# Optimization experiments

Measured on AMD Instinct MI355X. Metric: run time of the kernel, lower is better.

The kernel has to match this reference:

```python
import jax, jax.numpy as jnp
import numpy as np

B, S, F = 16, 511, 128           # batch, input seq len, n_features
D, H, NB = 512, 8, 6             # embedding_dim, n_heads, n_blocks
DH = D // H                      # d_head
MLP = 4 * D                      # mlp_ratio=4 hard-coded in FxtBlock
OUT = 1                          # out_d
T = S + 1                        # tokens incl. cls
EPS = 1e-5                       # torch LayerNorm default eps


def pos_emb(seq_len, d):
    # matches get_positional_embeddings: sin for even j, cos for odd j (with j-1 exponent)
    i = np.arange(seq_len, dtype=np.float32)[:, None]
    j = np.arange(d)
    je = np.where(j % 2 == 0, j, j - 1).astype(np.float32)
    ang = i / (10000.0 ** (je / d))
    pe = np.where(j % 2 == 0, np.sin(ang), np.cos(ang))
    return jnp.asarray(pe, jnp.float32)


def layernorm(x, g, b):
    m = jnp.mean(x, axis=-1, keepdims=True)
    v = jnp.mean((x - m) ** 2, axis=-1, keepdims=True)
    return (x - m) * jax.lax.rsqrt(v + EPS) * g + b


def setup_inputs() -> dict:
    key = jax.random.key(0)
    ks = jax.random.split(key, 12)
    g = lambda k, shape: jax.random.normal(k, shape, jnp.float32) * 0.02
    return {
        "src": jax.random.normal(ks[0], (B, S, F), jnp.float32),
        "emb_W": g(ks[1], (F, D)), "emb_b": jnp.zeros((D,), jnp.float32),
        "cls_tok": jax.random.uniform(ks[2], (1, D), jnp.float32),
        "ln1_g": jnp.ones((NB, D), jnp.float32), "ln1_b": jnp.zeros((NB, D), jnp.float32),
        "Wq": g(ks[3], (NB, H, DH, DH)), "bq": jnp.zeros((NB, H, DH), jnp.float32),
        "Wk": g(ks[4], (NB, H, DH, DH)), "bk": jnp.zeros((NB, H, DH), jnp.float32),
        "Wv": g(ks[5], (NB, H, DH, DH)), "bv": jnp.zeros((NB, H, DH), jnp.float32),
        "ln2_g": jnp.ones((NB, D), jnp.float32), "ln2_b": jnp.zeros((NB, D), jnp.float32),
        "W1": g(ks[6], (NB, D, MLP)), "b1": jnp.zeros((NB, MLP), jnp.float32),
        "W2": g(ks[7], (NB, MLP, D)), "b2": jnp.zeros((NB, D), jnp.float32),
        "head_W": g(ks[8], (D, OUT)), "head_b": jnp.zeros((OUT,), jnp.float32),
    }


def reference(src, emb_W, emb_b, cls_tok, ln1_g, ln1_b, Wq, bq, Wk, bk, Wv, bv,
              ln2_g, ln2_b, W1, b1, W2, b2, head_W, head_b):
    b = src.shape[0]
    x = src @ emb_W + emb_b                                    # [B,S,D]
    cls = jnp.broadcast_to(cls_tok[None], (b, 1, D))
    x = jnp.concatenate([cls, x], axis=1) + pos_emb(T, D)[None]  # [B,T,D]
    scale = 1.0 / jnp.sqrt(jnp.float32(DH))
    for i in range(NB):
        h = layernorm(x, ln1_g[i], ln1_b[i])
        hh = h.reshape(b, T, H, DH)
        q = jnp.einsum('bthd,hde->bhte', hh, Wq[i]) + bq[i][None, :, None, :]
        k = jnp.einsum('bthd,hde->bhte', hh, Wk[i]) + bk[i][None, :, None, :]
        v = jnp.einsum('bthd,hde->bhte', hh, Wv[i]) + bv[i][None, :, None, :]
        attn = jax.nn.softmax(jnp.einsum('bhse,bhte->bhst', q, k) * scale, axis=-1)
        o = jnp.einsum('bhst,bhte->bhse', attn, v)             # [B,H,T,DH]
        x = x + o.transpose(0, 2, 1, 3).reshape(b, T, D)
        h2 = layernorm(x, ln2_g[i], ln2_b[i])
        x = x + (jax.nn.gelu(h2 @ W1[i] + b1[i], approximate=False) @ W2[i] + b2[i])
    return jax.nn.sigmoid(x[:, 0] @ head_W + head_b)           # [B,OUT]
```

## Files before the change

### kernel.cpp

```cpp
#include <hip/hip_runtime.h>
#include <hip/hip_bf16.h>
#include <math.h>

#define B 16
#define S 511
#define F 128
#define D 512
#define H 8
#define NB 6
#define DH 64
#define MLPD 2048
#define T 512
#define EPS 1e-5f

typedef unsigned short ushort;
typedef __attribute__((ext_vector_type(8))) short short8;
typedef __attribute__((ext_vector_type(4))) float floatx4;

__device__ __forceinline__ ushort f2bf(float f) {
    union { float f; unsigned u; } cv; cv.f = f;
    unsigned r = (cv.u + 0x7fff + ((cv.u >> 16) & 1)) >> 16;
    return (ushort)r;
}

__global__ void castsrc_kernel(const float* __restrict__ src, ushort* __restrict__ srcb) {
    int row = blockIdx.x;
    int t = row & (T - 1), b = row >> 9;
    int tid = threadIdx.x;
    ushort v = 0;
    if (t > 0) v = f2bf(src[((size_t)b * S + (t - 1)) * F + tid]);
    srcb[(size_t)row * F + tid] = v;
}

__global__ void wtrans_kernel(const float* __restrict__ W,
                              ushort* __restrict__ Wt,
                              int K, int N) {
    int kb = blockIdx.x * 32, nb = blockIdx.y * 32, mat = blockIdx.z;
    __shared__ float tile[32][33];
    int tid = threadIdx.x;
    int c = tid & 31, r0 = tid >> 5;
    const float* Wm = W + (size_t)mat * K * N;
    ushort* Wtm = Wt + (size_t)mat * K * N;
    #pragma unroll
    for (int l = 0; l < 4; ++l) {
        int r = r0 + l * 8;
        tile[r][c] = Wm[(size_t)(kb + r) * N + nb + c];
    }
    __syncthreads();
    #pragma unroll
    for (int l = 0; l < 4; ++l) {
        int r = r0 + l * 8;
        Wtm[(size_t)(nb + r) * K + kb + c] = f2bf(tile[c][r]);
    }
}

__global__ void wtransq_kernel(const float* __restrict__ Wq, const float* __restrict__ Wk,
                               const float* __restrict__ Wv,
                               ushort* __restrict__ WqT, ushort* __restrict__ WkT,
                               ushort* __restrict__ WvT) {
    int mat = blockIdx.x;
    int which = blockIdx.y;
    const float* W = (which == 0 ? Wq : which == 1 ? Wk : Wv) + (size_t)mat * 4096;
    ushort* O = (which == 0 ? WqT : which == 1 ? WkT : WvT) + (size_t)mat * 4096;
    __shared__ float t[64][65];
    int tid = threadIdx.x;
    int r0 = tid >> 6, c = tid & 63;
    #pragma unroll
    for (int l = 0; l < 16; ++l) {
        int row = r0 * 16 + l;
        t[row][c] = W[row * 64 + c];
    }
    __syncthreads();
    #pragma unroll
    for (int l = 0; l < 16; ++l) {
        int row = r0 * 16 + l;
        O[row * 64 + c] = f2bf(t[c][row]);
    }
}

__device__ __forceinline__ void gload_lds16(const ushort* g, ushort* l) {
    __builtin_amdgcn_global_load_lds((const __attribute__((address_space(1))) unsigned int*)g,
                                     (__attribute__((address_space(3))) unsigned int*)l,
                                     16, 0, 0);
}

__global__ __launch_bounds__(256) void embed_gemm(const ushort* __restrict__ A,
                                                  const ushort* __restrict__ Bt,
                                                  const float* __restrict__ emb_b,
                                                  const float* __restrict__ cls_tok,
                                                  float* __restrict__ x) {
    __shared__ ushort As[64 * 32];
    __shared__ ushort Bs[64 * 32];
    int tid = threadIdx.x;
    int lane = tid & 63;
    int w = __builtin_amdgcn_readfirstlane(tid >> 6);
    int quad = lane >> 4, l15 = lane & 15;
    int wr = (w >> 1) * 32, wc = (w & 1) * 32;
    int m0 = blockIdx.x * 64, n0 = blockIdx.y * 64;

    floatx4 acc[2][2];
    #pragma unroll
    for (int i = 0; i < 2; ++i)
        #pragma unroll
        for (int j = 0; j < 2; ++j) acc[i][j] = (floatx4)0.f;

    int lrow = lane >> 2;
    int lk = (lane & 3) * 8;
    const ushort* Ag = A + (size_t)(m0 + 16 * w + lrow) * F + lk;
    const ushort* Bg = Bt + (size_t)(n0 + 16 * w + lrow) * F + lk;
    ushort* AsW = &As[16 * w * 32];
    ushort* BsW = &Bs[16 * w * 32];
    int fa = l15 * 32 + quad * 8;

    for (int kt = 0; kt < F; kt += 32) {
        gload_lds16(Ag + kt, AsW);
        gload_lds16(Bg + kt, BsW);
        __syncthreads();
        short8 af[2], bf[2];
        #pragma unroll
        for (int i = 0; i < 2; ++i) af[i] = *(const short8*)&As[(wr + 16 * i) * 32 + fa];
        #pragma unroll
        for (int j = 0; j < 2; ++j) bf[j] = *(const short8*)&Bs[(wc + 16 * j) * 32 + fa];
        #pragma unroll
        for (int i = 0; i < 2; ++i)
            #pragma unroll
            for (int j = 0; j < 2; ++j)
                acc[i][j] = __builtin_amdgcn_mfma_f32_16x16x32_bf16(af[i], bf[j], acc[i][j], 0, 0, 0);
        __syncthreads();
    }

    const float LOG1E4 = 9.210340371976184f;
    int rbase = (lane >> 4) * 4;
    int cidx = lane & 15;
    #pragma unroll
    for (int j = 0; j < 2; ++j) {
        int gc = n0 + wc + 16 * j + cidx;
        float je = (float)(gc & ~1);
        float freq = expf(-(je / (float)D) * LOG1E4);
        float ebv = emb_b[gc];
        float clsv = cls_tok[gc];
        bool odd = (gc & 1);
        #pragma unroll
        for (int i = 0; i < 2; ++i) {
            int gr = m0 + wr + 16 * i + rbase;
            #pragma unroll
            for (int reg = 0; reg < 4; ++reg) {
                int row = gr + reg;
                int t = row & (T - 1);
                float ang = (float)t * freq;
                float pe = odd ? cosf(ang) : sinf(ang);
                float val = (t == 0) ? (clsv + pe) : (acc[i][j][reg] + ebv + pe);
                x[(size_t)row * D + gc] = val;
            }
        }
    }
}

__global__ __launch_bounds__(256) void ln_kernel(const float* __restrict__ xin,
                                                 const float* __restrict__ g,
                                                 const float* __restrict__ bb,
                                                 ushort* __restrict__ out) {
    int lane = threadIdx.x & 63;
    int row = blockIdx.x * 4 + (threadIdx.x >> 6);
    const float* xr = xin + (size_t)row * D + lane * 8;
    float4 a0 = *(const float4*)xr;
    float4 a1 = *(const float4*)(xr + 4);
    float s = a0.x + a0.y + a0.z + a0.w + a1.x + a1.y + a1.z + a1.w;
    #pragma unroll
    for (int off = 1; off < 64; off <<= 1) s += __shfl_xor(s, off);
    float mean = s * (1.0f / (float)D);
    float d0 = a0.x - mean, d1 = a0.y - mean, d2 = a0.z - mean, d3 = a0.w - mean;
    float d4 = a1.x - mean, d5 = a1.y - mean, d6 = a1.z - mean, d7 = a1.w - mean;
    float sq = d0*d0 + d1*d1 + d2*d2 + d3*d3 + d4*d4 + d5*d5 + d6*d6 + d7*d7;
    #pragma unroll
    for (int off = 1; off < 64; off <<= 1) sq += __shfl_xor(sq, off);
    float rstd = rsqrtf(sq * (1.0f / (float)D) + EPS);
    const float* gp = g + lane * 8;
    const float* bp = bb + lane * 8;
    float4 g0 = *(const float4*)gp, g1 = *(const float4*)(gp + 4);
    float4 b0 = *(const float4*)bp, b1 = *(const float4*)(bp + 4);
    short8 o;
    o[0] = (short)f2bf(d0 * rstd * g0.x + b0.x);
    o[1] = (short)f2bf(d1 * rstd * g0.y + b0.y);
    o[2] = (short)f2bf(d2 * rstd * g0.z + b0.z);
    o[3] = (short)f2bf(d3 * rstd * g0.w + b0.w);
    o[4] = (short)f2bf(d4 * rstd * g1.x + b1.x);
    o[5] = (short)f2bf(d5 * rstd * g1.y + b1.y);
    o[6] = (short)f2bf(d6 * rstd * g1.z + b1.z);
    o[7] = (short)f2bf(d7 * rstd * g1.w + b1.w);
    *(short8*)(out + (size_t)row * D + lane * 8) = o;
}

__global__ __launch_bounds__(256) void ln_fuse_kernel(float* __restrict__ x,
                                                      const float* __restrict__ p0,
                                                      const float* __restrict__ p1,
                                                      const float* __restrict__ g,
                                                      const float* __restrict__ bb,
                                                      ushort* __restrict__ out) {
    int lane = threadIdx.x & 63;
    int row = blockIdx.x * 4 + (threadIdx.x >> 6);
    size_t base = (size_t)row * D + lane * 8;
    float* xr = x + base;
    float4 a0 = *(const float4*)xr;
    float4 a1 = *(const float4*)(xr + 4);
    float4 q0 = *(const float4*)(p0 + base);
    float4 q1 = *(const float4*)(p0 + base + 4);
    float4 r0v = *(const float4*)(p1 + base);
    float4 r1v = *(const float4*)(p1 + base + 4);
    a0.x += q0.x + r0v.x; a0.y += q0.y + r0v.y; a0.z += q0.z + r0v.z; a0.w += q0.w + r0v.w;
    a1.x += q1.x + r1v.x; a1.y += q1.y + r1v.y; a1.z += q1.z + r1v.z; a1.w += q1.w + r1v.w;
    *(float4*)xr = a0;
    *(float4*)(xr + 4) = a1;
    float s = a0.x + a0.y + a0.z + a0.w + a1.x + a1.y + a1.z + a1.w;
    #pragma unroll
    for (int off = 1; off < 64; off <<= 1) s += __shfl_xor(s, off);
    float mean = s * (1.0f / (float)D);
    float d0 = a0.x - mean, d1 = a0.y - mean, d2 = a0.z - mean, d3 = a0.w - mean;
    float d4 = a1.x - mean, d5 = a1.y - mean, d6 = a1.z - mean, d7 = a1.w - mean;
    float sq = d0*d0 + d1*d1 + d2*d2 + d3*d3 + d4*d4 + d5*d5 + d6*d6 + d7*d7;
    #pragma unroll
    for (int off = 1; off < 64; off <<= 1) sq += __shfl_xor(sq, off);
    float rstd = rsqrtf(sq * (1.0f / (float)D) + EPS);
    const float* gp = g + lane * 8;
    const float* bp = bb + lane * 8;
    float4 g0 = *(const float4*)gp, g1 = *(const float4*)(gp + 4);
    float4 b0 = *(const float4*)bp, b1 = *(const float4*)(bp + 4);
    short8 o;
    o[0] = (short)f2bf(d0 * rstd * g0.x + b0.x);
    o[1] = (short)f2bf(d1 * rstd * g0.y + b0.y);
    o[2] = (short)f2bf(d2 * rstd * g0.z + b0.z);
    o[3] = (short)f2bf(d3 * rstd * g0.w + b0.w);
    o[4] = (short)f2bf(d4 * rstd * g1.x + b1.x);
    o[5] = (short)f2bf(d5 * rstd * g1.y + b1.y);
    o[6] = (short)f2bf(d6 * rstd * g1.z + b1.z);
    o[7] = (short)f2bf(d7 * rstd * g1.w + b1.w);
    *(short8*)(out + (size_t)row * D + lane * 8) = o;
}

__global__ __launch_bounds__(256) void qkv_kernel(
        const ushort* __restrict__ hb,
        const ushort* __restrict__ WqT, const float* __restrict__ bq,
        const ushort* __restrict__ WkT, const float* __restrict__ bk,
        const ushort* __restrict__ WvT, const float* __restrict__ bv,
        ushort* __restrict__ qo, ushort* __restrict__ ko, ushort* __restrict__ vTo) {
    int m0 = blockIdx.x * 128;
    int hh = blockIdx.y;
    int tid = threadIdx.x;
    int lane = tid & 63;
    int w = __builtin_amdgcn_readfirstlane(tid >> 6);
    int quad = lane >> 4, l15 = lane & 15;

    short8 af[2][2];
    #pragma unroll
    for (int mt = 0; mt < 2; ++mt) {
        const ushort* ab = hb + (size_t)(m0 + w * 32 + mt * 16 + l15) * D + hh * DH + quad * 8;
        af[mt][0] = *(const short8*)(ab);
        af[mt][1] = *(const short8*)(ab + 32);
    }

    floatx4 acc[3][2][4];
    #pragma unroll
    for (int xo = 0; xo < 3; ++xo)
        #pragma unroll
        for (int mt = 0; mt < 2; ++mt)
            #pragma unroll
            for (int nt = 0; nt < 4; ++nt) acc[xo][mt][nt] = (floatx4)0.f;

    #pragma unroll
    for (int xo = 0; xo < 3; ++xo) {
        const ushort* WT = (xo == 0 ? WqT : xo == 1 ? WkT : WvT) + (size_t)hh * 4096;
        #pragma unroll
        for (int nt = 0; nt < 4; ++nt) {
            const ushort* wb = WT + (size_t)(nt * 16 + l15) * 64 + quad * 8;
            short8 bf0 = *(const short8*)(wb);
            short8 bf1 = *(const short8*)(wb + 32);
            #pragma unroll
            for (int mt = 0; mt < 2; ++mt) {
                acc[xo][mt][nt] = __builtin_amdgcn_mfma_f32_16x16x32_bf16(af[mt][0], bf0, acc[xo][mt][nt], 0, 0, 0);
                acc[xo][mt][nt] = __builtin_amdgcn_mfma_f32_16x16x32_bf16(af[mt][1], bf1, acc[xo][mt][nt], 0, 0, 0);
            }
        }
    }

    int bb = m0 >> 9;
    int bh = bb * H + hh;
    #pragma unroll
    for (int mt = 0; mt < 2; ++mt) {
        int trow = m0 + w * 32 + mt * 16 + quad * 4;
        int tt = trow & (T - 1);
        #pragma unroll
        for (int nt = 0; nt < 4; ++nt) {
            int col = nt * 16 + l15;
            float bqv = bq[hh * DH + col];
            float bkv = bk[hh * DH + col];
            float bvv = bv[hh * DH + col];
            #pragma unroll
            for (int reg = 0; reg < 4; ++reg) {
                qo[((size_t)bh * T + tt + reg) * DH + col] = f2bf(acc[0][mt][nt][reg] + bqv);
                ko[((size_t)bh * T + tt + reg) * DH + col] = f2bf(acc[1][mt][nt][reg] + bkv);
                vTo[((size_t)bh * DH + col) * T + tt + reg] = f2bf(acc[2][mt][nt][reg] + bvv);
            }
        }
    }
}

#define PSTRIDE 88
__global__ __launch_bounds__(256) void attn_kernel(const ushort* __restrict__ q,
                                                   const ushort* __restrict__ k,
                                                   const ushort* __restrict__ vT,
                                                   float* __restrict__ x) {
    int bh = blockIdx.x;
    int qt = blockIdx.y;
    int b = bh >> 3, hh = bh & 7;
    int tid = threadIdx.x;
    int lane = tid & 63;
    int w = __builtin_amdgcn_readfirstlane(tid >> 6);
    int quad = lane >> 4, l15 = lane & 15;

    __shared__ __align__(16) ushort smem[22016];
    ushort* Pw = smem + 16384 + w * (16 * PSTRIDE);

    const ushort* qbase = q + ((size_t)bh * T + qt * 64 + w * 16 + l15) * DH + quad * 8;
    short8 Qf0 = *(const short8*)(qbase);
    short8 Qf1 = *(const short8*)(qbase + 32);

    const ushort* kbase = k + (size_t)bh * T * DH;
    const ushort* vbase = vT + (size_t)bh * DH * T;

    int srow = lane >> 2;
    int scol = (lane & 3) * 8;
    const ushort* kg = kbase + (size_t)(w * 16 + srow) * DH + scol;
    const ushort* vg = vbase + (size_t)(w * 16 + srow) * T + scol;
    ushort* ldsK = smem + w * 16 * 32;
    ushort* ldsV = smem + 8192 + w * 16 * 32;

    float l_i[4] = {0.f, 0.f, 0.f, 0.f};
    floatx4 O[4];
    #pragma unroll
    for (int j = 0; j < 4; ++j) O[j] = (floatx4)0.f;

    gload_lds16(kg, ldsK);
    gload_lds16(kg + 32, ldsK + 2048);
    gload_lds16(vg, ldsV);
    gload_lds16(vg + 32, ldsV + 2048);
    __syncthreads();

    for (int kt = 0; kt < T / 64; ++kt) {
        int cur = kt & 1;
        if (kt < T / 64 - 1) {
            int nb = cur ^ 1;
            const ushort* kgn = kg + (size_t)(kt + 1) * 64 * DH;
            const ushort* vgn = vg + (kt + 1) * 64;
            gload_lds16(kgn, ldsK + nb * 4096);
            gload_lds16(kgn + 32, ldsK + nb * 4096 + 2048);
            gload_lds16(vgn, ldsV + nb * 4096);
            gload_lds16(vgn + 32, ldsV + nb * 4096 + 2048);
        }
        const ushort* Kc = smem + cur * 4096;
        const ushort* Vc = smem + 8192 + cur * 4096;

        floatx4 sc[4];
        #pragma unroll
        for (int j = 0; j < 4; ++j) {
            int ro = (j * 16 + l15) * 32 + quad * 8;
            short8 kf0 = *(const short8*)&Kc[ro];
            short8 kf1 = *(const short8*)&Kc[2048 + ro];
            floatx4 s4 = (floatx4)0.f;
            s4 = __builtin_amdgcn_mfma_f32_16x16x32_bf16(Qf0, kf0, s4, 0, 0, 0);
            s4 = __builtin_amdgcn_mfma_f32_16x16x32_bf16(Qf1, kf1, s4, 0, 0, 0);
            sc[j] = s4;
        }
        #pragma unroll
        for (int j = 0; j < 4; ++j) {
            #pragma unroll
            for (int r = 0; r < 4; ++r) {
                float p = __expf(sc[j][r] * 0.125f);
                ushort pb = f2bf(p);
                union { unsigned u; float f; } cv; cv.u = ((unsigned)pb) << 16;
                l_i[r] += cv.f;
                Pw[(quad * 4 + r) * PSTRIDE + j * 16 + l15] = pb;
            }
        }

        short8 af0 = *(const short8*)&Pw[l15 * PSTRIDE + quad * 8];
        short8 af1 = *(const short8*)&Pw[l15 * PSTRIDE + 32 + quad * 8];
        #pragma unroll
        for (int j = 0; j < 4; ++j) {
            int ro = (j * 16 + l15) * 32 + quad * 8;
            short8 vf0 = *(const short8*)&Vc[ro];
            short8 vf1 = *(const short8*)&Vc[2048 + ro];
            O[j] = __builtin_amdgcn_mfma_f32_16x16x32_bf16(af0, vf0, O[j], 0, 0, 0);
            O[j] = __builtin_amdgcn_mfma_f32_16x16x32_bf16(af1, vf1, O[j], 0, 0, 0);
        }
        __syncthreads();
    }

    #pragma unroll
    for (int r = 0; r < 4; ++r) {
        l_i[r] += __shfl_xor(l_i[r], 1);
        l_i[r] += __shfl_xor(l_i[r], 2);
        l_i[r] += __shfl_xor(l_i[r], 4);
        l_i[r] += __shfl_xor(l_i[r], 8);
    }

    float* Ow = (float*)smem + w * 16 * 68;
    #pragma unroll
    for (int r = 0; r < 4; ++r) {
        float rl = 1.0f / l_i[r];
        #pragma unroll
        for (int j = 0; j < 4; ++j)
            Ow[(quad * 4 + r) * 68 + j * 16 + l15] = O[j][r] * rl;
    }
    __syncthreads();
    int r4 = lane >> 4;
    int c16 = lane & 15;
    #pragma unroll
    for (int i = 0; i < 4; ++i) {
        int lrow = i * 4 + r4;
        float4 o = *(const float4*)&Ow[lrow * 68 + c16 * 4];
        int grow = qt * 64 + w * 16 + lrow;
        float* xp = &x[((size_t)(b * T) + grow) * D + hh * DH + c16 * 4];
        float4 xv = *(const float4*)xp;
        xv.x += o.x; xv.y += o.y; xv.z += o.z; xv.w += o.w;
        *(float4*)xp = xv;
    }
}

template<int MODE, int SPLIT>
__global__ __launch_bounds__(256) void mfma_gemm(const ushort* __restrict__ A,
                                                 const ushort* __restrict__ Bt,
                                                 const float* __restrict__ bias,
                                                 void* __restrict__ Cv,
                                                 int M, int N, int K) {
    __shared__ ushort As0[128 * 32];
    __shared__ ushort As1[128 * 32];
    __shared__ ushort Bs0[128 * 32];
    __shared__ ushort Bs1[128 * 32];
    int tid = threadIdx.x;
    int lane = tid & 63;
    int w = __builtin_amdgcn_readfirstlane(tid >> 6);
    int wr = (w >> 1) * 64, wc = (w & 1) * 64;
    int m0 = blockIdx.x * 128, n0 = blockIdx.y * 128;
    int kz = blockIdx.z;
    int kchunk = K / SPLIT;
    int k0 = kz * kchunk, k1 = k0 + kchunk;

    floatx4 acc[4][4];
    #pragma unroll
    for (int i = 0; i < 4; ++i)
        #pragma unroll
        for (int j = 0; j < 4; ++j) acc[i][j] = (floatx4)0.f;

    int lrow = lane >> 2;
    int lk = (lane & 3) * 8;
    const ushort* Ag = A + (size_t)(m0 + 32 * w + lrow) * K + lk;
    const ushort* Bg = Bt + (size_t)(n0 + 32 * w + lrow) * K + lk;
    ushort* As0W = &As0[(32 * w) * 32];
    ushort* As1W = &As1[(32 * w) * 32];
    ushort* Bs0W = &Bs0[(32 * w) * 32];
    ushort* Bs1W = &Bs1[(32 * w) * 32];
    int fa = (lane & 15) * 32 + (lane >> 4) * 8;

    for (int kt = k0; kt < k1; kt += 64) {
        gload_lds16(Ag + kt, As0W);
        gload_lds16(Ag + kt + (size_t)16 * K, As0W + 16 * 32);
        gload_lds16(Ag + kt + 32, As1W);
        gload_lds16(Ag + kt + 32 + (size_t)16 * K, As1W + 16 * 32);
        gload_lds16(Bg + kt, Bs0W);
        gload_lds16(Bg + kt + (size_t)16 * K, Bs0W + 16 * 32);
        gload_lds16(Bg + kt + 32, Bs1W);
        gload_lds16(Bg + kt + 32 + (size_t)16 * K, Bs1W + 16 * 32);
        __syncthreads();
        short8 af0[4], af1[4], bf0[4], bf1[4];
        #pragma unroll
        for (int i = 0; i < 4; ++i) {
            af0[i] = *(const short8*)&As0[(wr + 16 * i) * 32 + fa];
            af1[i] = *(const short8*)&As1[(wr + 16 * i) * 32 + fa];
        }
        #pragma unroll
        for (int j = 0; j < 4; ++j) {
            bf0[j] = *(const short8*)&Bs0[(wc + 16 * j) * 32 + fa];
            bf1[j] = *(const short8*)&Bs1[(wc + 16 * j) * 32 + fa];
        }
        #pragma unroll
        for (int i = 0; i < 4; ++i)
            #pragma unroll
            for (int j = 0; j < 4; ++j) {
                acc[i][j] = __builtin_amdgcn_mfma_f32_16x16x32_bf16(af0[i], bf0[j], acc[i][j], 0, 0, 0);
                acc[i][j] = __builtin_amdgcn_mfma_f32_16x16x32_bf16(af1[i], bf1[j], acc[i][j], 0, 0, 0);
            }
        __syncthreads();
    }

    int rbase = (lane >> 4) * 4;
    int cidx = lane & 15;
    if (MODE == 0) {
        ushort* C = (ushort*)Cv;
        #pragma unroll
        for (int i = 0; i < 4; ++i) {
            #pragma unroll
            for (int j = 0; j < 4; ++j) {
                int gc = n0 + wc + 16 * j + cidx;
                float bv = bias[gc];
                int gr = m0 + wr + 16 * i + rbase;
                #pragma unroll
                for (int reg = 0; reg < 4; ++reg) {
                    float val = acc[i][j][reg] + bv;
                    val = 0.5f * val * (1.0f + erff(val * 0.70710678118f));
                    C[(size_t)(gr + reg) * N + gc] = f2bf(val);
                }
            }
        }
    } else {
        float* C = (float*)Cv + (size_t)kz * M * N;
        #pragma unroll
        for (int i = 0; i < 4; ++i) {
            #pragma unroll
            for (int j = 0; j < 4; ++j) {
                int gc = n0 + wc + 16 * j + cidx;
                float bv = (kz == 0) ? bias[gc] : 0.f;
                int gr = m0 + wr + 16 * i + rbase;
                #pragma unroll
                for (int reg = 0; reg < 4; ++reg) {
                    C[(size_t)(gr + reg) * N + gc] = acc[i][j][reg] + bv;
                }
            }
        }
    }
}

__global__ void head_kernel(const float* __restrict__ x,
                            const float* __restrict__ p0,
                            const float* __restrict__ p1,
                            const float* __restrict__ hw,
                            const float* __restrict__ hb,
                            float* __restrict__ out) {
    int b = blockIdx.x;
    int tid = threadIdx.x;
    size_t idx = (size_t)b * T * D + tid;
    float s = (x[idx] + p0[idx] + p1[idx]) * hw[tid];
    #pragma unroll
    for (int off = 32; off > 0; off >>= 1) s += __shfl_down(s, off, 64);
    __shared__ float red[8];
    if ((tid & 63) == 0) red[tid >> 6] = s;
    __syncthreads();
    if (tid == 0) {
        float t = 0.f;
        #pragma unroll
        for (int i = 0; i < 8; ++i) t += red[i];
        out[b] = 1.0f / (1.0f + __expf(-(t + hb[0])));
    }
}

extern "C" void kernel_launch(void* const* d_in, const int* in_sizes, int n_in,
                              void* d_out, int out_size, void* d_ws, size_t ws_size,
                              hipStream_t stream) {
    const float* src     = (const float*)d_in[0];
    const float* emb_W   = (const float*)d_in[1];
    const float* emb_b   = (const float*)d_in[2];
    const float* cls_tok = (const float*)d_in[3];
    const float* ln1_g   = (const float*)d_in[4];
    const float* ln1_b   = (const float*)d_in[5];
    const float* Wq      = (const float*)d_in[6];
    const float* bq      = (const float*)d_in[7];
    const float* Wk      = (const float*)d_in[8];
    const float* bk      = (const float*)d_in[9];
    const float* Wv      = (const float*)d_in[10];
    const float* bv      = (const float*)d_in[11];
    const float* ln2_g   = (const float*)d_in[12];
    const float* ln2_b   = (const float*)d_in[13];
    const float* W1      = (const float*)d_in[14];
    const float* b1      = (const float*)d_in[15];
    const float* W2      = (const float*)d_in[16];
    const float* b2      = (const float*)d_in[17];
    const float* head_W  = (const float*)d_in[18];
    const float* head_b  = (const float*)d_in[19];

    const size_t NTOK = (size_t)B * T;
    char* wsb = (char*)d_ws;
    float*  x    = (float*)wsb;      wsb += NTOK * D * 4;
    float*  p01  = (float*)wsb;      wsb += NTOK * D * 4 * 2;
    ushort* hbuf = (ushort*)wsb;     wsb += NTOK * D * 2;
    ushort* q    = (ushort*)wsb;     wsb += NTOK * D * 2;
    ushort* k    = (ushort*)wsb;     wsb += NTOK * D * 2;
    ushort* vT   = (ushort*)wsb;     wsb += NTOK * D * 2;
    ushort* u    = (ushort*)wsb;     wsb += NTOK * MLPD * 2;
    ushort* W1t  = (ushort*)wsb;     wsb += (size_t)NB * D * MLPD * 2;
    ushort* W2t  = (ushort*)wsb;     wsb += (size_t)NB * D * MLPD * 2;
    ushort* WqT  = (ushort*)wsb;     wsb += (size_t)NB * H * DH * DH * 2;
    ushort* WkT  = (ushort*)wsb;     wsb += (size_t)NB * H * DH * DH * 2;
    ushort* WvT  = (ushort*)wsb;     wsb += (size_t)NB * H * DH * DH * 2;
    ushort* srcb = (ushort*)wsb;     wsb += NTOK * F * 2;
    ushort* embWt= (ushort*)wsb;     wsb += (size_t)F * D * 2;
    float* p0 = p01;
    float* p1 = p01 + NTOK * D;

    wtrans_kernel<<<dim3(D / 32, MLPD / 32, NB), 256, 0, stream>>>(W1, W1t, D, MLPD);
    wtrans_kernel<<<dim3(MLPD / 32, D / 32, NB), 256, 0, stream>>>(W2, W2t, MLPD, D);
    wtransq_kernel<<<dim3(NB * H, 3), 256, 0, stream>>>(Wq, Wk, Wv, WqT, WkT, WvT);
    wtrans_kernel<<<dim3(F / 32, D / 32, 1), 256, 0, stream>>>(emb_W, embWt, F, D);
    castsrc_kernel<<<B * T, F, 0, stream>>>(src, srcb);

    embed_gemm<<<dim3(B * T / 64, D / 64), 256, 0, stream>>>(srcb, embWt, emb_b, cls_tok, x);

    for (int i = 0; i < NB; ++i) {
        if (i == 0)
            ln_kernel<<<B * T / 4, 256, 0, stream>>>(x, ln1_g, ln1_b, hbuf);
        else
            ln_fuse_kernel<<<B * T / 4, 256, 0, stream>>>(x, p0, p1,
                ln1_g + i * D, ln1_b + i * D, hbuf);
        qkv_kernel<<<dim3(B * T / 128, H), 256, 0, stream>>>(hbuf,
            WqT + (size_t)i * H * DH * DH, bq + (size_t)i * H * DH,
            WkT + (size_t)i * H * DH * DH, bk + (size_t)i * H * DH,
            WvT + (size_t)i * H * DH * DH, bv + (size_t)i * H * DH,
            q, k, vT);
        attn_kernel<<<dim3(B * H, T / 64), 256, 0, stream>>>(q, k, vT, x);
        ln_kernel<<<B * T / 4, 256, 0, stream>>>(x, ln2_g + i * D, ln2_b + i * D, hbuf);
        mfma_gemm<0, 1><<<dim3(B * T / 128, MLPD / 128, 1), 256, 0, stream>>>(
            hbuf, W1t + (size_t)i * D * MLPD, b1 + (size_t)i * MLPD, u, B * T, MLPD, D);
        mfma_gemm<1, 2><<<dim3(B * T / 128, D / 128, 2), 256, 0, stream>>>(
            u, W2t + (size_t)i * MLPD * D, b2 + (size_t)i * D, p01, B * T, D, MLPD);
    }

    head_kernel<<<B, 512, 0, stream>>>(x, p0, p1, head_W, head_b, (float*)d_out);
}
```

Measured before the change: 890.6 us.

## Replace split-K W2 GEMM with narrower 128x64 tiles and use polynomial GELU

The second MLP GEMM no longer splits K in two. It writes a single partial buffer using 128x64 output tiles, which keeps the same block count (64x8 grid) without the second fp32 partial write and read. The LN-fuse and head kernels drop the second partial input. The erff-based GELU in the first GEMM epilogue is replaced by an Abramowitz-Stegun polynomial approximation with __expf, which cuts transcendental cost but adds small approximation error (around 1e-7 absolute).

```diff
diff --git a/kernel.cpp b/kernel.cpp
--- a/kernel.cpp
+++ b/kernel.cpp
@@ -21,6 +21,16 @@
     union { float f; unsigned u; } cv; cv.f = f;
     unsigned r = (cv.u + 0x7fff + ((cv.u >> 16) & 1)) >> 16;
     return (ushort)r;
+}
+
+__device__ __forceinline__ float fast_gelu(float x) {
+    float z = fabsf(x) * 0.70710678118f;
+    float t = 1.0f / (1.0f + 0.3275911f * z);
+    float p = ((((1.061405429f * t - 1.453152027f) * t + 1.421413741f) * t
+               - 0.284496736f) * t + 0.254829592f) * t;
+    float erfv = 1.0f - p * __expf(-z * z);
+    erfv = copysignf(erfv, x);
+    return 0.5f * x * (1.0f + erfv);
 }
 
 __global__ void castsrc_kernel(const float* __restrict__ src, ushort* __restrict__ srcb) {
@@ -193,7 +203,6 @@
 
 __global__ __launch_bounds__(256) void ln_fuse_kernel(float* __restrict__ x,
                                                       const float* __restrict__ p0,
-                                                      const float* __restrict__ p1,
                                                       const float* __restrict__ g,
                                                       const float* __restrict__ bb,
                                                       ushort* __restrict__ out) {
@@ -205,10 +214,8 @@
     float4 a1 = *(const float4*)(xr + 4);
     float4 q0 = *(const float4*)(p0 + base);
     float4 q1 = *(const float4*)(p0 + base + 4);
-    float4 r0v = *(const float4*)(p1 + base);
-    float4 r1v = *(const float4*)(p1 + base + 4);
-    a0.x += q0.x + r0v.x; a0.y += q0.y + r0v.y; a0.z += q0.z + r0v.z; a0.w += q0.w + r0v.w;
-    a1.x += q1.x + r1v.x; a1.y += q1.y + r1v.y; a1.z += q1.z + r1v.z; a1.w += q1.w + r1v.w;
+    a0.x += q0.x; a0.y += q0.y; a0.z += q0.z; a0.w += q0.w;
+    a1.x += q1.x; a1.y += q1.y; a1.z += q1.z; a1.w += q1.w;
     *(float4*)xr = a0;
     *(float4*)(xr + 4) = a1;
     float s = a0.x + a0.y + a0.z + a0.w + a1.x + a1.y + a1.z + a1.w;
@@ -426,12 +433,11 @@
     }
 }
 
-template<int MODE, int SPLIT>
-__global__ __launch_bounds__(256) void mfma_gemm(const ushort* __restrict__ A,
-                                                 const ushort* __restrict__ Bt,
-                                                 const float* __restrict__ bias,
-                                                 void* __restrict__ Cv,
-                                                 int M, int N, int K) {
+__global__ __launch_bounds__(256) void mfma_gemm_gelu(const ushort* __restrict__ A,
+                                                      const ushort* __restrict__ Bt,
+                                                      const float* __restrict__ bias,
+                                                      ushort* __restrict__ C,
+                                                      int M, int N, int K) {
     __shared__ ushort As0[128 * 32];
     __shared__ ushort As1[128 * 32];
     __shared__ ushort Bs0[128 * 32];
@@ -441,9 +447,6 @@
     int w = __builtin_amdgcn_readfirstlane(tid >> 6);
     int wr = (w >> 1) * 64, wc = (w & 1) * 64;
     int m0 = blockIdx.x * 128, n0 = blockIdx.y * 128;
-    int kz = blockIdx.z;
-    int kchunk = K / SPLIT;
-    int k0 = kz * kchunk, k1 = k0 + kchunk;
 
     floatx4 acc[4][4];
     #pragma unroll
@@ -461,7 +464,7 @@
     ushort* Bs1W = &Bs1[(32 * w) * 32];
     int fa = (lane & 15) * 32 + (lane >> 4) * 8;
 
-    for (int kt = k0; kt < k1; kt += 64) {
+    for (int kt = 0; kt < K; kt += 64) {
         gload_lds16(Ag + kt, As0W);
         gload_lds16(Ag + kt + (size_t)16 * K, As0W + 16 * 32);
         gload_lds16(Ag + kt + 32, As1W);
@@ -494,36 +497,94 @@
 
     int rbase = (lane >> 4) * 4;
     int cidx = lane & 15;
-    if (MODE == 0) {
-        ushort* C = (ushort*)Cv;
+    #pragma unroll
+    for (int i = 0; i < 4; ++i) {
+        #pragma unroll
+        for (int j = 0; j < 4; ++j) {
+            int gc = n0 + wc + 16 * j + cidx;
+            float bv = bias[gc];
+            int gr = m0 + wr + 16 * i + rbase;
+            #pragma unroll
+            for (int reg = 0; reg < 4; ++reg) {
+                float val = fast_gelu(acc[i][j][reg] + bv);
+                C[(size_t)(gr + reg) * N + gc] = f2bf(val);
+            }
+        }
+    }
+}
+
+__global__ __launch_bounds__(256) void mfma_gemm_p(const ushort* __restrict__ A,
+                                                   const ushort* __restrict__ Bt,
+                                                   const float* __restrict__ bias,
+                                                   float* __restrict__ C,
+                                                   int M, int N, int K) {
+    __shared__ ushort As0[128 * 32];
+    __shared__ ushort As1[128 * 32];
+    __shared__ ushort Bs0[64 * 32];
+    __shared__ ushort Bs1[64 * 32];
+    int tid = threadIdx.x;
+    int lane = tid & 63;
+    int w = __builtin_amdgcn_readfirstlane(tid >> 6);
+    int wr = (w >> 1) * 64, wc = (w & 1) * 32;
+    int m0 = blockIdx.x * 128, n0 = blockIdx.y * 64;
+
+    floatx4 acc[4][2];
+    #pragma unroll
+    for (int i = 0; i < 4; ++i)
+        #pragma unroll
+        for (int j = 0; j < 2; ++j) acc[i][j] = (floatx4)0.f;
+
+    int lrow = lane >> 2;
+    int lk = (lane & 3) * 8;
+    const ushort* Ag = A + (size_t)(m0 + 32 * w + lrow) * K + lk;
+    const ushort* Bg = Bt + (size_t)(n0 + 16 * w + lrow) * K + lk;
+    ushort* As0W = &As0[(32 * w) * 32];
+    ushort* As1W = &As1[(32 * w) * 32];
+    ushort* Bs0W = &Bs0[(16 * w) * 32];
+    ushort* Bs1W = &Bs1[(16 * w) * 32];
+    int fa = (lane & 15) * 32 + (lane >> 4) * 8;
+
+    for (int kt = 0; kt < K; kt += 64) {
+        gload_lds16(Ag + kt, As0W);
+        gload_lds16(Ag + kt + (size_t)16 * K, As0W + 16 * 32);
+        gload_lds16(Ag + kt + 32, As1W);
+        gload_lds16(Ag + kt + 32 + (size_t)16 * K, As1W + 16 * 32);
+        gload_lds16(Bg + kt, Bs0W);
+        gload_lds16(Bg + kt + 32, Bs1W);
+        __syncthreads();
+        short8 af0[4], af1[4], bf0[2], bf1[2];
         #pragma unroll
         for (int i = 0; i < 4; ++i) {
-            #pragma unroll
-            for (int j = 0; j < 4; ++j) {
-                int gc = n0 + wc + 16 * j + cidx;
-                float bv = bias[gc];
-                int gr = m0 + wr + 16 * i + rbase;
-                #pragma unroll
-                for (int reg = 0; reg < 4; ++reg) {
-                    float val = acc[i][j][reg] + bv;
-                    val = 0.5f * val * (1.0f + erff(val * 0.70710678118f));
-                    C[(size_t)(gr + reg) * N + gc] = f2bf(val);
-                }
-            }
-        }
-    } else {
-        float* C = (float*)Cv + (size_t)kz * M * N;
-        #pragma unroll
-        for (int i = 0; i < 4; ++i) {
-            #pragma unroll
-            for (int j = 0; j < 4; ++j) {
-                int gc = n0 + wc + 16 * j + cidx;
-                float bv = (kz == 0) ? bias[gc] : 0.f;
-                int gr = m0 + wr + 16 * i + rbase;
-                #pragma unroll
-                for (int reg = 0; reg < 4; ++reg) {
-                    C[(size_t)(gr + reg) * N + gc] = acc[i][j][reg] + bv;
-                }
+            af0[i] = *(const short8*)&As0[(wr + 16 * i) * 32 + fa];
+            af1[i] = *(const short8*)&As1[(wr + 16 * i) * 32 + fa];
+        }
+        #pragma unroll
+        for (int j = 0; j < 2; ++j) {
+            bf0[j] = *(const short8*)&Bs0[(wc + 16 * j) * 32 + fa];
+            bf1[j] = *(const short8*)&Bs1[(wc + 16 * j) * 32 + fa];
+        }
+        #pragma unroll
+        for (int i = 0; i < 4; ++i)
+            #pragma unroll
+            for (int j = 0; j < 2; ++j) {
+                acc[i][j] = __builtin_amdgcn_mfma_f32_16x16x32_bf16(af0[i], bf0[j], acc[i][j], 0, 0, 0);
+                acc[i][j] = __builtin_amdgcn_mfma_f32_16x16x32_bf16(af1[i], bf1[j], acc[i][j], 0, 0, 0);
+            }
+        __syncthreads();
+    }
+
+    int rbase = (lane >> 4) * 4;
+    int cidx = lane & 15;
+    #pragma unroll
+    for (int i = 0; i < 4; ++i) {
+        #pragma unroll
+        for (int j = 0; j < 2; ++j) {
+            int gc = n0 + wc + 16 * j + cidx;
+            float bv = bias[gc];
+            int gr = m0 + wr + 16 * i + rbase;
+            #pragma unroll
+            for (int reg = 0; reg < 4; ++reg) {
+                C[(size_t)(gr + reg) * N + gc] = acc[i][j][reg] + bv;
             }
         }
     }
@@ -531,14 +592,13 @@
 
 __global__ void head_kernel(const float* __restrict__ x,
                             const float* __restrict__ p0,
-                            const float* __restrict__ p1,
                             const float* __restrict__ hw,
                             const float* __restrict__ hb,
                             float* __restrict__ out) {
     int b = blockIdx.x;
     int tid = threadIdx.x;
     size_t idx = (size_t)b * T * D + tid;
-    float s = (x[idx] + p0[idx] + p1[idx]) * hw[tid];
+    float s = (x[idx] + p0[idx]) * hw[tid];
     #pragma unroll
     for (int off = 32; off > 0; off >>= 1) s += __shfl_down(s, off, 64);
     __shared__ float red[8];
@@ -579,7 +639,7 @@
     const size_t NTOK = (size_t)B * T;
     char* wsb = (char*)d_ws;
     float*  x    = (float*)wsb;      wsb += NTOK * D * 4;
-    float*  p01  = (float*)wsb;      wsb += NTOK * D * 4 * 2;
+    float*  p0   = (float*)wsb;      wsb += NTOK * D * 4;
     ushort* hbuf = (ushort*)wsb;     wsb += NTOK * D * 2;
     ushort* q    = (ushort*)wsb;     wsb += NTOK * D * 2;
     ushort* k    = (ushort*)wsb;     wsb += NTOK * D * 2;
@@ -592,8 +652,6 @@
     ushort* WvT  = (ushort*)wsb;     wsb += (size_t)NB * H * DH * DH * 2;
     ushort* srcb = (ushort*)wsb;     wsb += NTOK * F * 2;
     ushort* embWt= (ushort*)wsb;     wsb += (size_t)F * D * 2;
-    float* p0 = p01;
-    float* p1 = p01 + NTOK * D;
 
     wtrans_kernel<<<dim3(D / 32, MLPD / 32, NB), 256, 0, stream>>>(W1, W1t, D, MLPD);
     wtrans_kernel<<<dim3(MLPD / 32, D / 32, NB), 256, 0, stream>>>(W2, W2t, MLPD, D);
@@ -607,7 +665,7 @@
         if (i == 0)
             ln_kernel<<<B * T / 4, 256, 0, stream>>>(x, ln1_g, ln1_b, hbuf);
         else
-            ln_fuse_kernel<<<B * T / 4, 256, 0, stream>>>(x, p0, p1,
+            ln_fuse_kernel<<<B * T / 4, 256, 0, stream>>>(x, p0,
                 ln1_g + i * D, ln1_b + i * D, hbuf);
         qkv_kernel<<<dim3(B * T / 128, H), 256, 0, stream>>>(hbuf,
             WqT + (size_t)i * H * DH * DH, bq + (size_t)i * H * DH,
@@ -616,11 +674,11 @@
             q, k, vT);
         attn_kernel<<<dim3(B * H, T / 64), 256, 0, stream>>>(q, k, vT, x);
         ln_kernel<<<B * T / 4, 256, 0, stream>>>(x, ln2_g + i * D, ln2_b + i * D, hbuf);
-        mfma_gemm<0, 1><<<dim3(B * T / 128, MLPD / 128, 1), 256, 0, stream>>>(
+        mfma_gemm_gelu<<<dim3(B * T / 128, MLPD / 128), 256, 0, stream>>>(
             hbuf, W1t + (size_t)i * D * MLPD, b1 + (size_t)i * MLPD, u, B * T, MLPD, D);
-        mfma_gemm<1, 2><<<dim3(B * T / 128, D / 128, 2), 256, 0, stream>>>(
-            u, W2t + (size_t)i * MLPD * D, b2 + (size_t)i * D, p01, B * T, D, MLPD);
-    }
-
-    head_kernel<<<B, 512, 0, stream>>>(x, p0, p1, head_W, head_b, (float*)d_out);
-}
+        mfma_gemm_p<<<dim3(B * T / 128, D / 64), 256, 0, stream>>>(
+            u, W2t + (size_t)i * MLPD * D, b2 + (size_t)i * D, p0, B * T, D, MLPD);
+    }
+
+    head_kernel<<<B, 512, 0, stream>>>(x, p0, head_W, head_b, (float*)d_out);
+}
```

Result: no change. 891.5 us (+0.1%).
